# Kernel optimization log

Measured on AMD Instinct MI355X. Metric: run time of the kernel, lower is better.

## Reference

```python
import jax, jax.numpy as jnp
import numpy as np

HIDDEN = 4096
N_EXPERTS = 128
TOP_K = 8
N_GROUP = 8
TOPK_GROUP = 4
ROUTED_SCALE = 1.0
NORM_TOPK = True
T = 32768


def setup_inputs() -> dict:
    key = jax.random.key(0)
    k1, k2, k3 = jax.random.split(key, 3)
    hidden_states = jax.random.normal(k1, (T, HIDDEN), dtype=jnp.float32)
    weight = jax.random.normal(k2, (N_EXPERTS, HIDDEN), dtype=jnp.float32) * 0.02
    e_score_correction_bias = jax.random.normal(k3, (N_EXPERTS,), dtype=jnp.float32) * 0.1
    return {"hidden_states": hidden_states, "weight": weight,
            "e_score_correction_bias": e_score_correction_bias}


def reference(hidden_states, weight, e_score_correction_bias):
    # GLM4-MoE top-k router: linear -> sigmoid -> bias-corrected grouped top-k
    x = hidden_states.reshape(-1, HIDDEN)
    router_logits = jnp.einsum('th,eh->te', x, weight)          # [T, E]
    scores = jax.nn.sigmoid(router_logits)                      # [T, E]
    scores_for_choice = scores + e_score_correction_bias[None, :]

    per_group = N_EXPERTS // N_GROUP
    g = scores_for_choice.reshape(-1, N_GROUP, per_group)       # [T, G, E/G]
    # group score = sum of top-2 expert scores within each group
    group_scores = jax.lax.top_k(g, 2)[0].sum(axis=-1)          # [T, G]
    group_idx = jax.lax.top_k(group_scores, TOPK_GROUP)[1]      # [T, topk_group]
    group_mask = jax.nn.one_hot(group_idx, N_GROUP, dtype=scores.dtype).sum(axis=1)  # [T, G]
    score_mask = jnp.repeat(group_mask, per_group, axis=-1)     # [T, E]
    masked_scores = jnp.where(score_mask > 0, scores_for_choice, 0.0)

    topk_indices = jax.lax.top_k(masked_scores, TOP_K)[1]       # [T, top_k]
    topk_weights = jnp.take_along_axis(scores, topk_indices, axis=1)  # gather raw (un-biased) scores
    if NORM_TOPK:
        denom = topk_weights.sum(axis=-1, keepdims=True) + 1e-20
        topk_weights = topk_weights / denom
    topk_weights = topk_weights * ROUTED_SCALE
    return topk_indices, topk_weights
```

## Files before the change

### kernel.cpp

```cpp
#include <hip/hip_runtime.h>
#include <math.h>

#define T_TOKENS 32768
#define HIDDEN   4096
#define NEXP     128
#define TM       64
#define BK       32
#define NSTAGE   (HIDDEN / BK)
#define A_SHORTS   (3 * 4 * 512)
#define B_BASE_SH  A_SHORTS
#define B_SHORTS   (3 * 8 * 512)
#define LDS_SHORTS (A_SHORTS + B_SHORTS)
#define A_PLANE_SH (4 * 512)
#define B_PLANE_SH (8 * 512)
#define SC_STRIDE  129
#define B_CHUNK_BYTES (B_SHORTS * 2)
#define WS_BYTES ((size_t)NSTAGE * B_CHUNK_BYTES)

typedef short bf16x8 __attribute__((ext_vector_type(8)));
typedef short bf16x4 __attribute__((ext_vector_type(4)));
typedef float f32x4  __attribute__((ext_vector_type(4)));

__device__ __forceinline__ unsigned short f2bf(float f) {
    unsigned u = __float_as_uint(f);
    u += 0x7FFF + ((u >> 16) & 1);
    return (unsigned short)(u >> 16);
}
__device__ __forceinline__ float bf2f(unsigned short h) {
    return __uint_as_float(((unsigned)h) << 16);
}
__device__ __forceinline__ void split3(float x, unsigned short& b0,
                                       unsigned short& b1, unsigned short& b2) {
    b0 = f2bf(x);
    float r1 = x - bf2f(b0);
    b1 = f2bf(r1);
    float r2 = r1 - bf2f(b1);
    b2 = f2bf(r2);
}

__global__ __launch_bounds__(256) void presplit_w(
    const float* __restrict__ w, short* __restrict__ ws16)
{
    const int g = blockIdx.x * 256 + threadIdx.x;
    const int l = g & 63;
    const int t = (g >> 6) & 7;
    const int s = g >> 9;
    const int e  = t * 16 + (l & 15);
    const int kb = s * BK + ((l >> 4) & 3) * 8;
    const float* src = w + (size_t)e * HIDDEN + kb;
    float4 v0 = *(const float4*)(src);
    float4 v1 = *(const float4*)(src + 4);
    float vv[8] = {v0.x, v0.y, v0.z, v0.w, v1.x, v1.y, v1.z, v1.w};
    unsigned short h0[8], h1[8], h2[8];
#pragma unroll
    for (int j = 0; j < 8; ++j) split3(vv[j], h0[j], h1[j], h2[j]);
    const size_t base = ((size_t)s * 24 + t) * 64 + l;
    bf16x8 o0 = {(short)h0[0],(short)h0[1],(short)h0[2],(short)h0[3],
                 (short)h0[4],(short)h0[5],(short)h0[6],(short)h0[7]};
    bf16x8 o1 = {(short)h1[0],(short)h1[1],(short)h1[2],(short)h1[3],
                 (short)h1[4],(short)h1[5],(short)h1[6],(short)h1[7]};
    bf16x8 o2 = {(short)h2[0],(short)h2[1],(short)h2[2],(short)h2[3],
                 (short)h2[4],(short)h2[5],(short)h2[6],(short)h2[7]};
    *(bf16x8*)(ws16 + (base + 0 * 8 * 64) * 8) = o0;
    *(bf16x8*)(ws16 + (base + 1 * 8 * 64) * 8) = o1;
    *(bf16x8*)(ws16 + (base + 2 * 8 * 64) * 8) = o2;
}

__global__ __launch_bounds__(512, 4) void glm4_router_mfma(
    const float* __restrict__ x, const short* __restrict__ wsplit,
    const float* __restrict__ bias, float* __restrict__ out)
{
    __shared__ __align__(16) short lds[LDS_SHORTS];

    const int tid  = threadIdx.x;
    const int wid  = tid >> 6;
    const int lane = tid & 63;
    const int rt_base = (wid & 1) * 2;
    const int ct_base = (wid >> 1) * 2;
    const int tok_base = blockIdx.x * TM;

    const int arow = tid >> 3;
    const int aq   = tid & 7;
    const float* xrow = x + (size_t)(tok_base + arow) * HIDDEN + aq * 4;
    const int awr = ((arow >> 4) * 64 + ((arow & 15) | ((aq >> 1) << 4))) * 8
                    + (aq & 1) * 4;

    f32x4 acc[2][2];
    double accd[2][2][4];
#pragma unroll
    for (int r = 0; r < 2; ++r)
#pragma unroll
        for (int c = 0; c < 2; ++c) {
            acc[r][c] = (f32x4){0.f, 0.f, 0.f, 0.f};
#pragma unroll
            for (int v = 0; v < 4; ++v) accd[r][c][v] = 0.0;
        }

    float4 cx = *(const float4*)(xrow);

    for (int s = 0; s < NSTAGE; ++s) {
        if (s) __syncthreads();

        {
            const char* gsrc = (const char*)wsplit + (size_t)s * B_CHUNK_BYTES + tid * 16;
            char* ldst = (char*)lds + B_BASE_SH * 2 + tid * 16;
#pragma unroll
            for (int i = 0; i < 3; ++i) {
                __builtin_amdgcn_global_load_lds(
                    (const __attribute__((address_space(1))) unsigned*)(gsrc + i * 8192),
                    (__attribute__((address_space(3))) unsigned*)(ldst + i * 8192),
                    16, 0, 0);
            }
        }

        float4 nx = cx;
        if (s + 1 < NSTAGE) nx = *(const float4*)(xrow + (size_t)(s + 1) * BK);

        {
            float vv[4] = {cx.x, cx.y, cx.z, cx.w};
            unsigned short h0[4], h1[4], h2[4];
#pragma unroll
            for (int j = 0; j < 4; ++j) split3(vv[j], h0[j], h1[j], h2[j]);
            *(bf16x4*)(&lds[0 * A_PLANE_SH + awr]) =
                (bf16x4){(short)h0[0], (short)h0[1], (short)h0[2], (short)h0[3]};
            *(bf16x4*)(&lds[1 * A_PLANE_SH + awr]) =
                (bf16x4){(short)h1[0], (short)h1[1], (short)h1[2], (short)h1[3]};
            *(bf16x4*)(&lds[2 * A_PLANE_SH + awr]) =
                (bf16x4){(short)h2[0], (short)h2[1], (short)h2[2], (short)h2[3]};
        }
        __syncthreads();

        {
            bf16x8 A[3][2], B[3][2];
#pragma unroll
            for (int p = 0; p < 3; ++p)
#pragma unroll
                for (int r = 0; r < 2; ++r)
                    A[p][r] = *(const bf16x8*)(
                        &lds[p * A_PLANE_SH + ((rt_base + r) * 64 + lane) * 8]);
#pragma unroll
            for (int p = 0; p < 3; ++p)
#pragma unroll
                for (int c = 0; c < 2; ++c)
                    B[p][c] = *(const bf16x8*)(
                        &lds[B_BASE_SH + p * B_PLANE_SH + ((ct_base + c) * 64 + lane) * 8]);
#pragma unroll
            for (int r = 0; r < 2; ++r)
#pragma unroll
                for (int c = 0; c < 2; ++c) {
                    acc[r][c] = __builtin_amdgcn_mfma_f32_16x16x32_bf16(A[0][r], B[0][c], acc[r][c], 0, 0, 0);
                    acc[r][c] = __builtin_amdgcn_mfma_f32_16x16x32_bf16(A[0][r], B[1][c], acc[r][c], 0, 0, 0);
                    acc[r][c] = __builtin_amdgcn_mfma_f32_16x16x32_bf16(A[1][r], B[0][c], acc[r][c], 0, 0, 0);
                    acc[r][c] = __builtin_amdgcn_mfma_f32_16x16x32_bf16(A[0][r], B[2][c], acc[r][c], 0, 0, 0);
                    acc[r][c] = __builtin_amdgcn_mfma_f32_16x16x32_bf16(A[2][r], B[0][c], acc[r][c], 0, 0, 0);
                    acc[r][c] = __builtin_amdgcn_mfma_f32_16x16x32_bf16(A[1][r], B[1][c], acc[r][c], 0, 0, 0);
                }
        }

        if ((s & 3) == 3) {
#pragma unroll
            for (int r = 0; r < 2; ++r)
#pragma unroll
                for (int c = 0; c < 2; ++c) {
#pragma unroll
                    for (int v = 0; v < 4; ++v) accd[r][c][v] += (double)acc[r][c][v];
                    acc[r][c] = (f32x4){0.f, 0.f, 0.f, 0.f};
                }
        }
        cx = nx;
    }

    __syncthreads();
    float* sc = (float*)lds;
#pragma unroll
    for (int r = 0; r < 2; ++r)
#pragma unroll
        for (int c = 0; c < 2; ++c) {
#pragma unroll
            for (int v = 0; v < 4; ++v) {
                const int tokl = (rt_base + r) * 16 + (lane >> 4) * 4 + v;
                const int e    = (ct_base + c) * 16 + (lane & 15);
                const float lg = (float)accd[r][c][v];
                const float sg = (float)(1.0 / (1.0 + exp(-(double)lg)));
                sc[tokl * SC_STRIDE + e] = sg + bias[e];
            }
        }
    __syncthreads();

    if (tid < TM) {
        const float* scp = sc + tid * SC_STRIDE;

        float gsc[8];
#pragma unroll
        for (int g = 0; g < 8; ++g) {
            float m1 = -1e30f, m2 = -1e30f;
#pragma unroll
            for (int j = 0; j < 16; ++j) {
                const float v = scp[g * 16 + j];
                if (v > m1) { m2 = m1; m1 = v; }
                else if (v > m2) { m2 = v; }
            }
            gsc[g] = m1 + m2;
        }

        unsigned gmask = 0;
#pragma unroll
        for (int p = 0; p < 4; ++p) {
            float best = -1e30f; int bi = 0;
#pragma unroll
            for (int g = 0; g < 8; ++g) {
                const bool taken = (gmask >> g) & 1u;
                if (!taken && gsc[g] > best) { best = gsc[g]; bi = g; }
            }
            gmask |= 1u << bi;
        }

        unsigned long long chosen0 = 0ull, chosen1 = 0ull;
        int   idxs[8];
        float wts[8];
#pragma unroll
        for (int p = 0; p < 8; ++p) {
            float best = -1e30f; int bi = 0;
            for (int e = 0; e < NEXP; ++e) {
                const bool sel = (gmask >> (e >> 4)) & 1u;
                const float v = sel ? scp[e] : 0.0f;
                const bool ch = (e < 64) ? ((chosen0 >> e) & 1ull)
                                         : ((chosen1 >> (e - 64)) & 1ull);
                if (!ch && v > best) { best = v; bi = e; }
            }
            if (bi < 64) chosen0 |= 1ull << bi; else chosen1 |= 1ull << (bi - 64);
            idxs[p] = bi;
            wts[p] = scp[bi] - bias[bi];
        }

        float denom = 0.0f;
#pragma unroll
        for (int p = 0; p < 8; ++p) denom += wts[p];
        denom += 1e-20f;

        const size_t row = (size_t)(tok_base + tid) * 8;
        float* outI = out;
        float* outW = out + (size_t)T_TOKENS * 8;
#pragma unroll
        for (int p = 0; p < 8; ++p) {
            outI[row + p] = (float)idxs[p];
            outW[row + p] = wts[p] / denom;
        }
    }
}

extern "C" void kernel_launch(void* const* d_in, const int* in_sizes, int n_in,
                              void* d_out, int out_size, void* d_ws, size_t ws_size,
                              hipStream_t stream) {
    const float* x    = (const float*)d_in[0];
    const float* w    = (const float*)d_in[1];
    const float* bias = (const float*)d_in[2];
    float* out = (float*)d_out;
    short* ws16 = (short*)d_ws;

    presplit_w<<<dim3(NSTAGE * 8 * 64 / 256), 256, 0, stream>>>(w, ws16);
    glm4_router_mfma<<<dim3(T_TOKENS / TM), 512, 0, stream>>>(x, ws16, bias, out);
}
```

Baseline: 285.7 us.

## Double-buffer A and B LDS tiles to overlap loads with MFMA compute

Converts the single-buffered K loop into a two-stage ping-pong pipeline. The next B chunk is loaded into LDS and the next A tile is split into bf16 planes while MFMAs run on the current buffer, so each stage needs one barrier instead of two. The A load mapping is also changed so each thread writes a contiguous LDS slot, and x is prefetched two stages ahead. LDS use doubles to about 72 KB per block, which may lower how many blocks fit on a CU.

```diff
diff --git a/kernel.cpp b/kernel.cpp
--- a/kernel.cpp
+++ b/kernel.cpp
@@ -7,14 +7,17 @@
 #define TM       64
 #define BK       32
 #define NSTAGE   (HIDDEN / BK)
-#define A_SHORTS   (3 * 4 * 512)
-#define B_BASE_SH  A_SHORTS
-#define B_SHORTS   (3 * 8 * 512)
-#define LDS_SHORTS (A_SHORTS + B_SHORTS)
-#define A_PLANE_SH (4 * 512)
-#define B_PLANE_SH (8 * 512)
-#define SC_STRIDE  129
-#define B_CHUNK_BYTES (B_SHORTS * 2)
+
+#define A_BUF_SH      6144
+#define B_BASE_SH     (2 * A_BUF_SH)
+#define B_BUF_SH      12288
+#define LDS_SHORTS    (B_BASE_SH + 2 * B_BUF_SH)
+#define B_BASE_BYTES  (B_BASE_SH * 2)
+#define B_BUF_BYTES   (B_BUF_SH * 2)
+#define A_PLANE_SH    2048
+#define B_PLANE_SH    4096
+#define SC_STRIDE     129
+#define B_CHUNK_BYTES B_BUF_BYTES
 #define WS_BYTES ((size_t)NSTAGE * B_CHUNK_BYTES)
 
 typedef short bf16x8 __attribute__((ext_vector_type(8)));
@@ -79,11 +82,12 @@
     const int ct_base = (wid >> 1) * 2;
     const int tok_base = blockIdx.x * TM;
 
-    const int arow = tid >> 3;
-    const int aq   = tid & 7;
-    const float* xrow = x + (size_t)(tok_base + arow) * HIDDEN + aq * 4;
-    const int awr = ((arow >> 4) * 64 + ((arow & 15) | ((aq >> 1) << 4))) * 8
-                    + (aq & 1) * 4;
+    const int al = (tid >> 1) & 63;
+    const int at = tid >> 7;
+    const int arow = at * 16 + (al & 15);
+    const int akoff = ((al >> 4) & 3) * 8 + (tid & 1) * 4;
+    const float* xsrc = x + (size_t)(tok_base + arow) * HIDDEN + akoff;
+    const int awr = tid * 4;
 
     f32x4 acc[2][2];
     double accd[2][2][4];
@@ -96,79 +100,99 @@
             for (int v = 0; v < 4; ++v) accd[r][c][v] = 0.0;
         }
 
-    float4 cx = *(const float4*)(xrow);
-
-    for (int s = 0; s < NSTAGE; ++s) {
-        if (s) __syncthreads();
-
-        {
-            const char* gsrc = (const char*)wsplit + (size_t)s * B_CHUNK_BYTES + tid * 16;
-            char* ldst = (char*)lds + B_BASE_SH * 2 + tid * 16;
-#pragma unroll
-            for (int i = 0; i < 3; ++i) {
-                __builtin_amdgcn_global_load_lds(
-                    (const __attribute__((address_space(1))) unsigned*)(gsrc + i * 8192),
-                    (__attribute__((address_space(3))) unsigned*)(ldst + i * 8192),
-                    16, 0, 0);
-            }
-        }
-
-        float4 nx = cx;
-        if (s + 1 < NSTAGE) nx = *(const float4*)(xrow + (size_t)(s + 1) * BK);
-
-        {
-            float vv[4] = {cx.x, cx.y, cx.z, cx.w};
-            unsigned short h0[4], h1[4], h2[4];
-#pragma unroll
-            for (int j = 0; j < 4; ++j) split3(vv[j], h0[j], h1[j], h2[j]);
-            *(bf16x4*)(&lds[0 * A_PLANE_SH + awr]) =
-                (bf16x4){(short)h0[0], (short)h0[1], (short)h0[2], (short)h0[3]};
-            *(bf16x4*)(&lds[1 * A_PLANE_SH + awr]) =
-                (bf16x4){(short)h1[0], (short)h1[1], (short)h1[2], (short)h1[3]};
-            *(bf16x4*)(&lds[2 * A_PLANE_SH + awr]) =
-                (bf16x4){(short)h2[0], (short)h2[1], (short)h2[2], (short)h2[3]};
-        }
-        __syncthreads();
-
-        {
-            bf16x8 A[3][2], B[3][2];
-#pragma unroll
-            for (int p = 0; p < 3; ++p)
-#pragma unroll
-                for (int r = 0; r < 2; ++r)
-                    A[p][r] = *(const bf16x8*)(
-                        &lds[p * A_PLANE_SH + ((rt_base + r) * 64 + lane) * 8]);
-#pragma unroll
-            for (int p = 0; p < 3; ++p)
-#pragma unroll
-                for (int c = 0; c < 2; ++c)
-                    B[p][c] = *(const bf16x8*)(
-                        &lds[B_BASE_SH + p * B_PLANE_SH + ((ct_base + c) * 64 + lane) * 8]);
-#pragma unroll
-            for (int r = 0; r < 2; ++r)
-#pragma unroll
-                for (int c = 0; c < 2; ++c) {
-                    acc[r][c] = __builtin_amdgcn_mfma_f32_16x16x32_bf16(A[0][r], B[0][c], acc[r][c], 0, 0, 0);
-                    acc[r][c] = __builtin_amdgcn_mfma_f32_16x16x32_bf16(A[0][r], B[1][c], acc[r][c], 0, 0, 0);
-                    acc[r][c] = __builtin_amdgcn_mfma_f32_16x16x32_bf16(A[1][r], B[0][c], acc[r][c], 0, 0, 0);
-                    acc[r][c] = __builtin_amdgcn_mfma_f32_16x16x32_bf16(A[0][r], B[2][c], acc[r][c], 0, 0, 0);
-                    acc[r][c] = __builtin_amdgcn_mfma_f32_16x16x32_bf16(A[2][r], B[0][c], acc[r][c], 0, 0, 0);
-                    acc[r][c] = __builtin_amdgcn_mfma_f32_16x16x32_bf16(A[1][r], B[1][c], acc[r][c], 0, 0, 0);
-                }
-        }
-
-        if ((s & 3) == 3) {
-#pragma unroll
-            for (int r = 0; r < 2; ++r)
-#pragma unroll
-                for (int c = 0; c < 2; ++c) {
-#pragma unroll
-                    for (int v = 0; v < 4; ++v) accd[r][c][v] += (double)acc[r][c][v];
-                    acc[r][c] = (f32x4){0.f, 0.f, 0.f, 0.f};
-                }
-        }
-        cx = nx;
+#define GLDS_B(S, BUF) do {                                                    \
+    const char* gsrc_ = (const char*)wsplit + (size_t)(S) * B_CHUNK_BYTES + tid * 16; \
+    char* ldst_ = (char*)lds + B_BASE_BYTES + (BUF) * B_BUF_BYTES + tid * 16;  \
+    __builtin_amdgcn_global_load_lds(                                          \
+        (const __attribute__((address_space(1))) unsigned*)(gsrc_),            \
+        (__attribute__((address_space(3))) unsigned*)(ldst_), 16, 0, 0);       \
+    __builtin_amdgcn_global_load_lds(                                          \
+        (const __attribute__((address_space(1))) unsigned*)(gsrc_ + 8192),     \
+        (__attribute__((address_space(3))) unsigned*)(ldst_ + 8192), 16, 0, 0);\
+    __builtin_amdgcn_global_load_lds(                                          \
+        (const __attribute__((address_space(1))) unsigned*)(gsrc_ + 16384),    \
+        (__attribute__((address_space(3))) unsigned*)(ldst_ + 16384), 16, 0, 0);\
+} while (0)
+
+#define SPLIT_A(XV, BUF) do {                                                  \
+    unsigned short h0_[4], h1_[4], h2_[4];                                     \
+    split3((XV).x, h0_[0], h1_[0], h2_[0]);                                    \
+    split3((XV).y, h0_[1], h1_[1], h2_[1]);                                    \
+    split3((XV).z, h0_[2], h1_[2], h2_[2]);                                    \
+    split3((XV).w, h0_[3], h1_[3], h2_[3]);                                    \
+    short* ab_ = &lds[(BUF) * A_BUF_SH + awr];                                 \
+    *(bf16x4*)(ab_ + 0 * A_PLANE_SH) =                                         \
+        (bf16x4){(short)h0_[0], (short)h0_[1], (short)h0_[2], (short)h0_[3]};  \
+    *(bf16x4*)(ab_ + 1 * A_PLANE_SH) =                                         \
+        (bf16x4){(short)h1_[0], (short)h1_[1], (short)h1_[2], (short)h1_[3]};  \
+    *(bf16x4*)(ab_ + 2 * A_PLANE_SH) =                                         \
+        (bf16x4){(short)h2_[0], (short)h2_[1], (short)h2_[2], (short)h2_[3]};  \
+} while (0)
+
+#define COMPUTE(S, BUF) do {                                                   \
+    bf16x8 Af[3][2], Bf[3][2];                                                 \
+    _Pragma("unroll")                                                          \
+    for (int p = 0; p < 3; ++p) {                                              \
+        _Pragma("unroll")                                                      \
+        for (int r = 0; r < 2; ++r)                                            \
+            Af[p][r] = *(const bf16x8*)(&lds[(BUF) * A_BUF_SH + p * A_PLANE_SH \
+                                             + ((rt_base + r) * 64 + lane) * 8]); \
+        _Pragma("unroll")                                                      \
+        for (int c = 0; c < 2; ++c)                                            \
+            Bf[p][c] = *(const bf16x8*)(&lds[B_BASE_SH + (BUF) * B_BUF_SH      \
+                                             + p * B_PLANE_SH                  \
+                                             + ((ct_base + c) * 64 + lane) * 8]); \
+    }                                                                          \
+    _Pragma("unroll")                                                          \
+    for (int r = 0; r < 2; ++r) {                                              \
+        _Pragma("unroll")                                                      \
+        for (int c = 0; c < 2; ++c) {                                          \
+            acc[r][c] = __builtin_amdgcn_mfma_f32_16x16x32_bf16(Af[0][r], Bf[0][c], acc[r][c], 0, 0, 0); \
+            acc[r][c] = __builtin_amdgcn_mfma_f32_16x16x32_bf16(Af[0][r], Bf[1][c], acc[r][c], 0, 0, 0); \
+            acc[r][c] = __builtin_amdgcn_mfma_f32_16x16x32_bf16(Af[1][r], Bf[0][c], acc[r][c], 0, 0, 0); \
+            acc[r][c] = __builtin_amdgcn_mfma_f32_16x16x32_bf16(Af[0][r], Bf[2][c], acc[r][c], 0, 0, 0); \
+            acc[r][c] = __builtin_amdgcn_mfma_f32_16x16x32_bf16(Af[2][r], Bf[0][c], acc[r][c], 0, 0, 0); \
+            acc[r][c] = __builtin_amdgcn_mfma_f32_16x16x32_bf16(Af[1][r], Bf[1][c], acc[r][c], 0, 0, 0); \
+        }                                                                      \
+    }                                                                          \
+    if (((S) & 3) == 3) {                                                      \
+        _Pragma("unroll")                                                      \
+        for (int r = 0; r < 2; ++r)                                            \
+            _Pragma("unroll")                                                  \
+            for (int c = 0; c < 2; ++c) {                                      \
+                _Pragma("unroll")                                              \
+                for (int v = 0; v < 4; ++v) accd[r][c][v] += (double)acc[r][c][v]; \
+                acc[r][c] = (f32x4){0.f, 0.f, 0.f, 0.f};                       \
+            }                                                                  \
+    }                                                                          \
+} while (0)
+
+    float4 xA, xB;
+    {
+        float4 x0v = *(const float4*)(xsrc);
+        GLDS_B(0, 0);
+        xA = *(const float4*)(xsrc + BK);
+        SPLIT_A(x0v, 0);
     }
+    __syncthreads();
+
+#define BODY(S, BUF, XC, XL) do {                                              \
+    GLDS_B((S) + 1, (BUF) ^ 1);                                                \
+    {                                                                          \
+        int s2_ = (S) + 2; if (s2_ > NSTAGE - 1) s2_ = NSTAGE - 1;             \
+        XL = *(const float4*)(xsrc + (size_t)s2_ * BK);                        \
+    }                                                                          \
+    SPLIT_A(XC, (BUF) ^ 1);                                                    \
+    COMPUTE(S, BUF);                                                           \
+    __syncthreads();                                                           \
+} while (0)
+
+    for (int s = 0; s < NSTAGE - 2; s += 2) {
+        BODY(s, 0, xA, xB);
+        BODY(s + 1, 1, xB, xA);
+    }
+    BODY(NSTAGE - 2, 0, xA, xB);
+    COMPUTE(NSTAGE - 1, 1);
 
     __syncthreads();
     float* sc = (float*)lds;
```

New measurement: 282.3 us. Within noise of the previous version (-1.2%).
